# Kernel optimization log

Hardware: AMD Instinct MI355X
Metric: run time of the kernel (lower is better)

Reference implementation:

```python
import jax, jax.numpy as jnp
import numpy as np

B, C, M, T = 2, 512, 16, 128
H = 8
D = C // H  # 64, divisible by 4 for 2D RoPE
G = C // 4  # GroupNorm groups = 128
S = M * T


def group_norm(x, scale, bias, groups=G, eps=1e-5):
    b, c, m, t = x.shape
    xg = x.reshape(b, groups, c // groups, m, t)
    mu = xg.mean(axis=(2, 3, 4), keepdims=True)
    var = xg.var(axis=(2, 3, 4), keepdims=True)
    xn = ((xg - mu) * jax.lax.rsqrt(var + eps)).reshape(b, c, m, t)
    return xn * scale[None, :, None, None] + bias[None, :, None, None]


def dwsep_conv(x, dw, pw):
    # depthwise 3x3 (groups=C) then pointwise 1x1
    y = jax.lax.conv_general_dilated(
        x, dw, window_strides=(1, 1), padding='SAME',
        dimension_numbers=('NCHW', 'HWIO', 'NCHW'), feature_group_count=x.shape[1])
    return jnp.einsum('bcmt,cd->bdmt', y, pw)


def rope2d(x):
    # x: [B,H,M,T,D]; first D/2 dims rotated by freq index m, last D/2 by time index t
    d = x.shape[-1]
    dh = d // 2
    q = dh // 2
    inv = 1.0 / (10000.0 ** (jnp.arange(q, dtype=jnp.float32) / q))

    def rot(v, ang):
        h = v.shape[-1] // 2
        v1, v2 = v[..., :h], v[..., h:]
        c, s = jnp.cos(ang), jnp.sin(ang)
        return jnp.concatenate([v1 * c - v2 * s, v1 * s + v2 * c], axis=-1)

    ang_f = jnp.arange(x.shape[2], dtype=jnp.float32)[:, None] * inv  # [M,q]
    ang_t = jnp.arange(x.shape[3], dtype=jnp.float32)[:, None] * inv  # [T,q]
    xf = rot(x[..., :dh], ang_f[:, None, :])  # broadcast over T
    xt = rot(x[..., dh:], ang_t)
    return jnp.concatenate([xf, xt], axis=-1)


def setup_inputs() -> dict:
    key = jax.random.key(0)
    ks = jax.random.split(key, 14)
    s = 0.02
    return {
        'x': jax.random.normal(ks[0], (B, C, M, T), jnp.float32),
        'lengths': jax.random.randint(ks[1], (B,), T // 2, T + 1),
        'gn_scale': jnp.ones((C,), jnp.float32),
        'gn_bias': jnp.zeros((C,), jnp.float32),
        'dw_q': jax.random.normal(ks[2], (3, 3, 1, C), jnp.float32) * s,
        'dw_k': jax.random.normal(ks[3], (3, 3, 1, C), jnp.float32) * s,
        'dw_v': jax.random.normal(ks[4], (3, 3, 1, C), jnp.float32) * s,
        'pw_q': jax.random.normal(ks[5], (C, C), jnp.float32) * s,
        'pw_k': jax.random.normal(ks[6], (C, C), jnp.float32) * s,
        'pw_v': jax.random.normal(ks[7], (C, C), jnp.float32) * s,
        'attn_w': jax.random.normal(ks[8], (C, C), jnp.float32) * s,
        'attn_b': jnp.zeros((C,), jnp.float32),
        'out_w': jax.random.normal(ks[9], (C, C), jnp.float32) * s,
        'out_b': jnp.zeros((C,), jnp.float32),
    }


def reference(x, lengths, gn_scale, gn_bias, dw_q, dw_k, dw_v, pw_q, pw_k, pw_v,
              attn_w, attn_b, out_w, out_b):
    residual = x
    xn = group_norm(x, gn_scale, gn_bias)

    def to_heads(y):  # [B,C,M,T] -> [B,H,M,T,D]
        return y.reshape(B, H, D, M, T).transpose(0, 1, 3, 4, 2)

    q = rope2d(to_heads(dwsep_conv(xn, dw_q, pw_q)))
    k = rope2d(to_heads(dwsep_conv(xn, dw_k, pw_k)))
    v = to_heads(dwsep_conv(xn, dw_v, pw_v))

    q = q.reshape(B, H, S, D)
    k = k.reshape(B, H, S, D)
    v = v.reshape(B, H, S, D)

    scores = jnp.einsum('bhsd,bhkd->bhsk', q, k) / np.sqrt(D).astype(np.float32)
    valid_t = jnp.arange(T)[None, :] < lengths[:, None]        # [B,T]
    valid = jnp.tile(valid_t, (1, M))                          # [B,S], token idx = m*T + t
    scores = jnp.where(valid[:, None, None, :], scores, jnp.float32(-1e9))
    attn = jax.nn.softmax(scores, axis=-1)
    o = jnp.einsum('bhsk,bhkd->bhsd', attn, v)                 # [B,H,S,D]

    o = o.transpose(0, 2, 1, 3).reshape(B, S, C)
    o = o @ attn_w + attn_b                                    # block output proj
    o = o.reshape(B, M, T, C).transpose(0, 3, 1, 2)            # [B,C,M,T]
    out = jnp.einsum('bcmt,cd->bdmt', o, out_w) + out_b[None, :, None, None]
    return residual + out
```

## Files before the change

kernel.cpp:

```cpp
#include <hip/hip_runtime.h>
#include <math.h>

#define CCH 512
#define SSQ 2048
#define MTOT 4096

typedef __bf16 bf16;
typedef __bf16 bf16x8 __attribute__((ext_vector_type(8)));
typedef __bf16 bf16x4 __attribute__((ext_vector_type(4)));
typedef float  f32x4  __attribute__((ext_vector_type(4)));

#define AS1 __attribute__((address_space(1)))
#define AS3 __attribute__((address_space(3)))
__device__ __forceinline__ void glds16(const void* g, void* l) {
    __builtin_amdgcn_global_load_lds((const AS1 void*)g, (AS3 void*)l, 16, 0, 0);
}

__global__ void gn_stats_kernel(const float* __restrict__ x,
                                float* __restrict__ mu, float* __restrict__ rstd) {
    __shared__ float s_sum[256], s_sq[256];
    int bg = blockIdx.x;
    long base = (long)bg * 8192;
    int tid = threadIdx.x;
    float sum = 0.f, sq = 0.f;
#pragma unroll
    for (int r = 0; r < 32; ++r) {
        float v = x[base + r*256 + tid];
        sum += v; sq += v*v;
    }
    s_sum[tid] = sum; s_sq[tid] = sq;
    __syncthreads();
    for (int off = 128; off > 0; off >>= 1) {
        if (tid < off) { s_sum[tid] += s_sum[tid+off]; s_sq[tid] += s_sq[tid+off]; }
        __syncthreads();
    }
    if (tid == 0) {
        float m = s_sum[0] * (1.f/8192.f);
        float v = s_sq[0]  * (1.f/8192.f) - m*m;
        mu[bg] = m;
        rstd[bg] = rsqrtf(v + 1e-5f);
    }
}

__global__ void wconv_kernel(const float* __restrict__ w0, const float* __restrict__ w1,
                             const float* __restrict__ w2, const float* __restrict__ w3,
                             const float* __restrict__ w4, bf16* __restrict__ out) {
    __shared__ float t[64][65];
    const float* srcs[5] = {w0, w1, w2, w3, w4};
    const float* W = srcs[blockIdx.z];
    bf16* D = out + (long)blockIdx.z * (CCH*CCH);
    int k0 = blockIdx.x*64, n0 = blockIdx.y*64;
    int tid = threadIdx.x;
    int cI = tid & 63, r4 = tid >> 6;
#pragma unroll
    for (int p = 0; p < 16; ++p) {
        int kr = p*4 + r4;
        t[kr][cI] = W[(long)(k0+kr)*CCH + n0 + cI];
    }
    __syncthreads();
#pragma unroll
    for (int p = 0; p < 16; ++p) {
        int nr = p*4 + r4;
        D[(long)(n0+nr)*CCH + k0 + cI] = (bf16)t[cI][nr];
    }
}

__global__ void tn_kernel(const float* __restrict__ x, const float* __restrict__ mu,
                          const float* __restrict__ rstd, const float* __restrict__ gsc,
                          const float* __restrict__ gbs, bf16* __restrict__ xnT) {
    __shared__ float t[64][65];
    int s0 = blockIdx.x*64, c0 = blockIdx.y*64, b = blockIdx.z;
    int tid = threadIdx.x;
    int cI = tid & 63, r4 = tid >> 6;
#pragma unroll
    for (int p = 0; p < 16; ++p) {
        int cr = p*4 + r4;
        t[cr][cI] = x[((long)(b*CCH + c0 + cr))*SSQ + s0 + cI];
    }
    __syncthreads();
#pragma unroll
    for (int p = 0; p < 16; ++p) {
        int sr = p*4 + r4;
        int c = c0 + cI;
        int g = b*128 + (c >> 2);
        float v = (t[cI][sr] - mu[g]) * rstd[g] * gsc[c] + gbs[c];
        xnT[((long)(b*SSQ + s0 + sr))*CCH + c] = (bf16)v;
    }
}

__global__ __launch_bounds__(256) void dw3_kernel(const bf16* __restrict__ xnT,
        const float* __restrict__ dwq, const float* __restrict__ dwk,
        const float* __restrict__ dwv,
        bf16* __restrict__ yq, bf16* __restrict__ yk, bf16* __restrict__ yv) {
    int tid = threadIdx.x;
    int cc = (tid & 63) * 8;
    int s  = blockIdx.x*4 + (tid >> 6);
    int sl = s & (SSQ-1);
    int b  = s >> 11;
    int m = sl >> 7, t = sl & 127;
    float aq[8] = {}, ak[8] = {}, av[8] = {};
#pragma unroll
    for (int di = 0; di < 3; ++di) {
        int m2 = m + di - 1;
        if ((unsigned)m2 >= 16u) continue;
#pragma unroll
        for (int dj = 0; dj < 3; ++dj) {
            int t2 = t + dj - 1;
            if ((unsigned)t2 >= 128u) continue;
            bf16x8 xv = *(const bf16x8*)(xnT + ((long)(b*SSQ + m2*128 + t2))*CCH + cc);
            int wi = (di*3 + dj)*CCH + cc;
#pragma unroll
            for (int i = 0; i < 8; ++i) {
                float xf = (float)xv[i];
                aq[i] += xf * dwq[wi+i];
                ak[i] += xf * dwk[wi+i];
                av[i] += xf * dwv[wi+i];
            }
        }
    }
    bf16x8 oq, ok, ov;
#pragma unroll
    for (int i = 0; i < 8; ++i) { oq[i] = (bf16)aq[i]; ok[i] = (bf16)ak[i]; ov[i] = (bf16)av[i]; }
    long o = (long)s*CCH + cc;
    *(bf16x8*)(yq + o) = oq;
    *(bf16x8*)(yk + o) = ok;
    *(bf16x8*)(yv + o) = ov;
}

template<int MODE>
__global__ __launch_bounds__(256) void gemm_bf16(const bf16* __restrict__ A,
        const bf16* __restrict__ Wt, const float* __restrict__ bias,
        const float* __restrict__ resid, void* __restrict__ outv) {
    __shared__ bf16 As[64*64];
    __shared__ bf16 Bs[64*64];
    int m0 = blockIdx.x*64, n0 = blockIdx.y*64;
    int tid = threadIdx.x, lane = tid & 63, wid = tid >> 6;
    int sw = wid & 1, nw = wid >> 1;
    int col = lane & 15, quad = lane >> 4;
    f32x4 acc[2][2] = {};

    const char* gA[2]; const char* gB[2];
    char* ldsA[2]; char* ldsB[2];
#pragma unroll
    for (int p = 0; p < 2; ++p) {
        int ci = wid*64 + lane + p*256;
        int row = ci >> 3;
        int c = (ci & 7) ^ (row & 7);
        gA[p] = (const char*)A  + ((long)(m0+row)*CCH + c*8)*2;
        gB[p] = (const char*)Wt + ((long)(n0+row)*CCH + c*8)*2;
        ldsA[p] = (char*)As + wid*1024 + p*4096;
        ldsB[p] = (char*)Bs + wid*1024 + p*4096;
    }
    int rowA = sw*32 + col, rowB = nw*32 + col;

    for (int k0 = 0; k0 < CCH; k0 += 64) {
        __syncthreads();
#pragma unroll
        for (int p = 0; p < 2; ++p) {
            glds16(gA[p] + k0*2, ldsA[p]);
            glds16(gB[p] + k0*2, ldsB[p]);
        }
        __syncthreads();
        bf16x8 af[2][2], bf[2][2];
#pragma unroll
        for (int mt = 0; mt < 2; ++mt) {
            int r = rowA + mt*16;
#pragma unroll
            for (int ks = 0; ks < 2; ++ks) {
                int c = (ks*4 + quad) ^ (r & 7);
                af[mt][ks] = *(const bf16x8*)((char*)As + r*128 + c*16);
            }
        }
#pragma unroll
        for (int nt = 0; nt < 2; ++nt) {
            int r = rowB + nt*16;
#pragma unroll
            for (int ks = 0; ks < 2; ++ks) {
                int c = (ks*4 + quad) ^ (r & 7);
                bf[nt][ks] = *(const bf16x8*)((char*)Bs + r*128 + c*16);
            }
        }
#pragma unroll
        for (int ks = 0; ks < 2; ++ks)
#pragma unroll
            for (int mt = 0; mt < 2; ++mt)
#pragma unroll
                for (int nt = 0; nt < 2; ++nt)
                    acc[mt][nt] = __builtin_amdgcn_mfma_f32_16x16x32_bf16(
                        af[mt][ks], bf[nt][ks], acc[mt][nt], 0,0,0);
    }
    int nb = n0 + nw*32;
    int mb = m0 + sw*32;
    if (MODE == 0 || MODE == 1) {
        bf16* outp = (bf16*)outv;
        float invf = __expf(-(float)col * 0.5756462732485114f);
        bool tHalf = (nb & 32) != 0;
        const float sc = (MODE == 0) ? 0.125f : 1.0f;
#pragma unroll
        for (int st = 0; st < 2; ++st)
#pragma unroll
            for (int r = 0; r < 4; ++r) {
                int row = mb + st*16 + quad*4 + r;
                int sl = row & (SSQ-1);
                float pos = tHalf ? (float)(sl & 127) : (float)(sl >> 7);
                float ang = pos * invf;
                float sn, cs;
                __sincosf(ang, &sn, &cs);
                float x1 = acc[st][0][r], x2 = acc[st][1][r];
                outp[(long)row*CCH + nb + col]      = (bf16)((x1*cs - x2*sn)*sc);
                outp[(long)row*CCH + nb + 16 + col] = (bf16)((x1*sn + x2*cs)*sc);
            }
    } else if (MODE == 2) {
        bf16* outp = (bf16*)outv;
#pragma unroll
        for (int st = 0; st < 2; ++st)
#pragma unroll
            for (int nt = 0; nt < 2; ++nt) {
                int n = nb + nt*16 + col;
                int row0 = mb + st*16 + quad*4;
                int b = row0 >> 11, sl0 = row0 & (SSQ-1);
                bf16x4 pk;
#pragma unroll
                for (int r = 0; r < 4; ++r) pk[r] = (bf16)acc[st][nt][r];
                *(bf16x4*)(outp + ((long)(b*CCH + n))*SSQ + sl0) = pk;
            }
    } else if (MODE == 3) {
        bf16* outp = (bf16*)outv;
#pragma unroll
        for (int nt = 0; nt < 2; ++nt) {
            int n = nb + nt*16 + col;
            float bv = bias[n];
#pragma unroll
            for (int st = 0; st < 2; ++st)
#pragma unroll
                for (int r = 0; r < 4; ++r)
                    outp[(long)(mb + st*16 + quad*4 + r)*CCH + n] = (bf16)(acc[st][nt][r] + bv);
        }
    } else {
        float* outp = (float*)outv;
#pragma unroll
        for (int st = 0; st < 2; ++st)
#pragma unroll
            for (int nt = 0; nt < 2; ++nt) {
                int n = nb + nt*16 + col;
                float bv = bias[n];
                int row0 = mb + st*16 + quad*4;
                int b = row0 >> 11, sl0 = row0 & (SSQ-1);
                long off = ((long)(b*CCH + n))*SSQ + sl0;
                float4 rr = *(const float4*)(resid + off);
                float4 o4;
                o4.x = acc[st][nt][0] + bv + rr.x;
                o4.y = acc[st][nt][1] + bv + rr.y;
                o4.z = acc[st][nt][2] + bv + rr.z;
                o4.w = acc[st][nt][3] + bv + rr.w;
                *(float4*)(outp + off) = o4;
            }
    }
}

#define KVROW 88
#define KVIMG (64*KVROW*2)
__global__ __launch_bounds__(256) void attn_kernel(
        const bf16* __restrict__ qb, const bf16* __restrict__ kb,
        const bf16* __restrict__ vb, const int* __restrict__ lengths,
        bf16* __restrict__ o) {
    __shared__ char KVs[2][2*KVIMG];
    __shared__ bf16 Ps[4][16*72];
    int b = blockIdx.z, h = blockIdx.y;
    int tid = threadIdx.x, wid = tid >> 6, lane = tid & 63;
    int col = lane & 15, quad = lane >> 4;
    int q0 = blockIdx.x*64 + wid*16;
    int lenb = lengths[b];

    const char* gp[4]; long gstep[4]; int ldsoff[4];
#pragma unroll
    for (int p = 0; p < 4; ++p) {
        int idx = tid + p*256;
        int isV = idx >> 9;
        int r = (idx >> 3) & 63;
        int c = idx & 7;
        if (!isV) { gp[p] = (const char*)kb + ((long)(b*SSQ + r))*1024 + h*128 + c*16; gstep[p] = 65536; }
        else      { gp[p] = (const char*)vb + ((long)(b*CCH + h*64 + r))*4096 + c*16;  gstep[p] = 128; }
        ldsoff[p] = isV*KVIMG + r*176 + c*16;
    }

    const bf16* qp = qb + (long)(b*SSQ)*CCH + h*64;
    bf16x8 qf[2];
#pragma unroll
    for (int dc = 0; dc < 2; ++dc)
        qf[dc] = *(const bf16x8*)(qp + (long)(q0 + col)*CCH + dc*32 + quad*8);

    f32x4 of[4] = {};
    float lsum = 0.f;
    bf16* pw = Ps[wid];

    bf16x8 sreg[4];
#pragma unroll
    for (int p = 0; p < 4; ++p) sreg[p] = *(const bf16x8*)(gp[p]);
#pragma unroll
    for (int p = 0; p < 4; ++p) *(bf16x8*)(KVs[0] + ldsoff[p]) = sreg[p];
    __syncthreads();

    for (int t = 0; t < 32; ++t) {
        int kt = t*64;
        const bf16* K = (const bf16*)KVs[t & 1];
        const bf16* V = (const bf16*)(KVs[t & 1] + KVIMG);
        if (t < 31) {
#pragma unroll
            for (int p = 0; p < 4; ++p)
                sreg[p] = *(const bf16x8*)(gp[p] + (long)(t+1)*gstep[p]);
        }
        f32x4 acc[4] = {};
#pragma unroll
        for (int sub = 0; sub < 4; ++sub)
#pragma unroll
            for (int dc = 0; dc < 2; ++dc) {
                bf16x8 kf = *(const bf16x8*)(K + (sub*16 + col)*KVROW + dc*32 + quad*8);
                acc[sub] = __builtin_amdgcn_mfma_f32_16x16x32_bf16(kf, qf[dc], acc[sub], 0,0,0);
            }
#pragma unroll
        for (int sub = 0; sub < 4; ++sub) {
            bf16x4 pk;
#pragma unroll
            for (int r = 0; r < 4; ++r) {
                int key = kt + sub*16 + quad*4 + r;
                float p = ((key & 127) < lenb) ? __expf(acc[sub][r]) : 0.f;
                lsum += p;
                pk[r] = (bf16)p;
            }
            *(bf16x4*)(pw + col*72 + sub*16 + quad*4) = pk;
        }
#pragma unroll
        for (int ks = 0; ks < 2; ++ks) {
            bf16x8 pf = *(const bf16x8*)(pw + col*72 + ks*32 + quad*8);
#pragma unroll
            for (int dt = 0; dt < 4; ++dt) {
                bf16x8 vf = *(const bf16x8*)(V + (dt*16 + col)*KVROW + ks*32 + quad*8);
                of[dt] = __builtin_amdgcn_mfma_f32_16x16x32_bf16(pf, vf, of[dt], 0,0,0);
            }
        }
        if (t < 31) {
            char* nb2 = KVs[(t + 1) & 1];
#pragma unroll
            for (int p = 0; p < 4; ++p) *(bf16x8*)(nb2 + ldsoff[p]) = sreg[p];
        }
        __syncthreads();
    }
    lsum += __shfl_xor(lsum, 16);
    lsum += __shfl_xor(lsum, 32);
    float invl = 1.f / lsum;
    float ir[4];
#pragma unroll
    for (int r = 0; r < 4; ++r) ir[r] = __shfl(invl, quad*4 + r);
    bf16* ob = o + (long)(b*SSQ + q0)*CCH + h*64;
#pragma unroll
    for (int dt = 0; dt < 4; ++dt)
#pragma unroll
        for (int r = 0; r < 4; ++r)
            ob[(long)(quad*4 + r)*CCH + dt*16 + col] = (bf16)(of[dt][r] * ir[r]);
}

extern "C" void kernel_launch(void* const* d_in, const int* in_sizes, int n_in,
                              void* d_out, int out_size, void* d_ws, size_t ws_size,
                              hipStream_t stream) {
    const float* x        = (const float*)d_in[0];
    const int*   lengths  = (const int*)  d_in[1];
    const float* gn_scale = (const float*)d_in[2];
    const float* gn_bias  = (const float*)d_in[3];
    const float* dw_q     = (const float*)d_in[4];
    const float* dw_k     = (const float*)d_in[5];
    const float* dw_v     = (const float*)d_in[6];
    const float* pw_q     = (const float*)d_in[7];
    const float* pw_k     = (const float*)d_in[8];
    const float* pw_v     = (const float*)d_in[9];
    const float* attn_w   = (const float*)d_in[10];
    const float* attn_b   = (const float*)d_in[11];
    const float* out_w    = (const float*)d_in[12];
    const float* out_b    = (const float*)d_in[13];
    float* out = (float*)d_out;

    char* w = (char*)d_ws;
    float* mu   = (float*)w;
    float* rstd = (float*)(w + 1024);
    bf16* wT    = (bf16*)(w + 4096);
    bf16* wTq = wT;
    bf16* wTk = wT + 1*CCH*CCH;
    bf16* wTv = wT + 2*CCH*CCH;
    bf16* wTa = wT + 3*CCH*CCH;
    bf16* wTo = wT + 4*CCH*CCH;
    bf16* xnT  = (bf16*)(w + 0x00300000);
    bf16* yqT  = (bf16*)(w + 0x00700000);
    bf16* ykT  = (bf16*)(w + 0x00B00000);
    bf16* yvT  = (bf16*)(w + 0x00F00000);
    bf16* qbf  = (bf16*)(w + 0x01300000);
    bf16* kbf  = (bf16*)(w + 0x01700000);
    bf16* vbf  = (bf16*)(w + 0x01B00000);
    bf16* obf  = (bf16*)(w + 0x01F00000);
    bf16* tmpb = (bf16*)(w + 0x02300000);

    gn_stats_kernel<<<256, 256, 0, stream>>>(x, mu, rstd);
    wconv_kernel<<<dim3(8,8,5), 256, 0, stream>>>(pw_q, pw_k, pw_v, attn_w, out_w, wT);
    tn_kernel<<<dim3(32,8,2), 256, 0, stream>>>(x, mu, rstd, gn_scale, gn_bias, xnT);
    dw3_kernel<<<MTOT/4, 256, 0, stream>>>(xnT, dw_q, dw_k, dw_v, yqT, ykT, yvT);

    dim3 gg(MTOT/64, CCH/64);
    gemm_bf16<0><<<gg, 256, 0, stream>>>(yqT, wTq, nullptr, nullptr, qbf);
    gemm_bf16<1><<<gg, 256, 0, stream>>>(ykT, wTk, nullptr, nullptr, kbf);
    gemm_bf16<2><<<gg, 256, 0, stream>>>(yvT, wTv, nullptr, nullptr, vbf);

    attn_kernel<<<dim3(SSQ/64, 8, 2), 256, 0, stream>>>(qbf, kbf, vbf, lengths, obf);

    gemm_bf16<3><<<gg, 256, 0, stream>>>(obf, wTa, attn_b, nullptr, tmpb);
    gemm_bf16<4><<<gg, 256, 0, stream>>>(tmpb, wTo, out_b, x, out);
}
```

Before: 179.8 us.

## Merge setup kernels, batch QKV GEMMs, and swizzle attention K/V tiles

```diff
diff --git a/kernel.cpp b/kernel.cpp
--- a/kernel.cpp
+++ b/kernel.cpp
@@ -16,52 +16,56 @@
     __builtin_amdgcn_global_load_lds((const AS1 void*)g, (AS3 void*)l, 16, 0, 0);
 }
 
-__global__ void gn_stats_kernel(const float* __restrict__ x,
-                                float* __restrict__ mu, float* __restrict__ rstd) {
-    __shared__ float s_sum[256], s_sq[256];
-    int bg = blockIdx.x;
-    long base = (long)bg * 8192;
+__global__ __launch_bounds__(256) void gnw_kernel(const float* __restrict__ x,
+        float* __restrict__ mu, float* __restrict__ rstd,
+        const float* __restrict__ w0, const float* __restrict__ w1,
+        const float* __restrict__ w2, const float* __restrict__ w3,
+        const float* __restrict__ w4, bf16* __restrict__ wT) {
+    __shared__ float smem[64*65];
     int tid = threadIdx.x;
-    float sum = 0.f, sq = 0.f;
-#pragma unroll
-    for (int r = 0; r < 32; ++r) {
-        float v = x[base + r*256 + tid];
-        sum += v; sq += v*v;
-    }
-    s_sum[tid] = sum; s_sq[tid] = sq;
-    __syncthreads();
-    for (int off = 128; off > 0; off >>= 1) {
-        if (tid < off) { s_sum[tid] += s_sum[tid+off]; s_sq[tid] += s_sq[tid+off]; }
-        __syncthreads();
-    }
-    if (tid == 0) {
-        float m = s_sum[0] * (1.f/8192.f);
-        float v = s_sq[0]  * (1.f/8192.f) - m*m;
-        mu[bg] = m;
-        rstd[bg] = rsqrtf(v + 1e-5f);
-    }
-}
-
-__global__ void wconv_kernel(const float* __restrict__ w0, const float* __restrict__ w1,
-                             const float* __restrict__ w2, const float* __restrict__ w3,
-                             const float* __restrict__ w4, bf16* __restrict__ out) {
-    __shared__ float t[64][65];
-    const float* srcs[5] = {w0, w1, w2, w3, w4};
-    const float* W = srcs[blockIdx.z];
-    bf16* D = out + (long)blockIdx.z * (CCH*CCH);
-    int k0 = blockIdx.x*64, n0 = blockIdx.y*64;
-    int tid = threadIdx.x;
-    int cI = tid & 63, r4 = tid >> 6;
-#pragma unroll
-    for (int p = 0; p < 16; ++p) {
-        int kr = p*4 + r4;
-        t[kr][cI] = W[(long)(k0+kr)*CCH + n0 + cI];
-    }
-    __syncthreads();
-#pragma unroll
-    for (int p = 0; p < 16; ++p) {
-        int nr = p*4 + r4;
-        D[(long)(n0+nr)*CCH + k0 + cI] = (bf16)t[cI][nr];
+    if (blockIdx.x < 256) {
+        float* s_sum = smem;
+        float* s_sq  = smem + 256;
+        int bg = blockIdx.x;
+        long base = (long)bg * 8192;
+        float sum = 0.f, sq = 0.f;
+#pragma unroll
+        for (int r = 0; r < 32; ++r) {
+            float v = x[base + r*256 + tid];
+            sum += v; sq += v*v;
+        }
+        s_sum[tid] = sum; s_sq[tid] = sq;
+        __syncthreads();
+        for (int off = 128; off > 0; off >>= 1) {
+            if (tid < off) { s_sum[tid] += s_sum[tid+off]; s_sq[tid] += s_sq[tid+off]; }
+            __syncthreads();
+        }
+        if (tid == 0) {
+            float m = s_sum[0] * (1.f/8192.f);
+            float v = s_sq[0]  * (1.f/8192.f) - m*m;
+            mu[bg] = m;
+            rstd[bg] = rsqrtf(v + 1e-5f);
+        }
+    } else {
+        int bid = blockIdx.x - 256;
+        int z = bid >> 6, r2 = bid & 63;
+        int k0 = (r2 >> 3)*64, n0 = (r2 & 7)*64;
+        const float* srcs[5] = {w0, w1, w2, w3, w4};
+        const float* W = srcs[z];
+        bf16* D = wT + (long)z * (CCH*CCH);
+        float (*t)[65] = (float(*)[65])smem;
+        int cI = tid & 63, r4 = tid >> 6;
+#pragma unroll
+        for (int p = 0; p < 16; ++p) {
+            int kr = p*4 + r4;
+            t[kr][cI] = W[(long)(k0+kr)*CCH + n0 + cI];
+        }
+        __syncthreads();
+#pragma unroll
+        for (int p = 0; p < 16; ++p) {
+            int nr = p*4 + r4;
+            D[(long)(n0+nr)*CCH + k0 + cI] = (bf16)t[cI][nr];
+        }
     }
 }
 
@@ -127,18 +131,12 @@
     *(bf16x8*)(yv + o) = ov;
 }
 
-template<int MODE>
-__global__ __launch_bounds__(256) void gemm_bf16(const bf16* __restrict__ A,
-        const bf16* __restrict__ Wt, const float* __restrict__ bias,
-        const float* __restrict__ resid, void* __restrict__ outv) {
-    __shared__ bf16 As[64*64];
-    __shared__ bf16 Bs[64*64];
-    int m0 = blockIdx.x*64, n0 = blockIdx.y*64;
+__device__ __forceinline__ void gemm_core(const bf16* __restrict__ A,
+        const bf16* __restrict__ Wt, int m0, int n0,
+        bf16* As, bf16* Bs, f32x4 acc[2][2]) {
     int tid = threadIdx.x, lane = tid & 63, wid = tid >> 6;
     int sw = wid & 1, nw = wid >> 1;
     int col = lane & 15, quad = lane >> 4;
-    f32x4 acc[2][2] = {};
-
     const char* gA[2]; const char* gB[2];
     char* ldsA[2]; char* ldsB[2];
 #pragma unroll
@@ -152,7 +150,6 @@
         ldsB[p] = (char*)Bs + wid*1024 + p*4096;
     }
     int rowA = sw*32 + col, rowB = nw*32 + col;
-
     for (int k0 = 0; k0 < CCH; k0 += 64) {
         __syncthreads();
 #pragma unroll
@@ -161,7 +158,7 @@
             glds16(gB[p] + k0*2, ldsB[p]);
         }
         __syncthreads();
-        bf16x8 af[2][2], bf[2][2];
+        bf16x8 af[2][2], bfr[2][2];
 #pragma unroll
         for (int mt = 0; mt < 2; ++mt) {
             int r = rowA + mt*16;
@@ -177,7 +174,7 @@
 #pragma unroll
             for (int ks = 0; ks < 2; ++ks) {
                 int c = (ks*4 + quad) ^ (r & 7);
-                bf[nt][ks] = *(const bf16x8*)((char*)Bs + r*128 + c*16);
+                bfr[nt][ks] = *(const bf16x8*)((char*)Bs + r*128 + c*16);
             }
         }
 #pragma unroll
@@ -187,15 +184,27 @@
 #pragma unroll
                 for (int nt = 0; nt < 2; ++nt)
                     acc[mt][nt] = __builtin_amdgcn_mfma_f32_16x16x32_bf16(
-                        af[mt][ks], bf[nt][ks], acc[mt][nt], 0,0,0);
-    }
-    int nb = n0 + nw*32;
-    int mb = m0 + sw*32;
-    if (MODE == 0 || MODE == 1) {
-        bf16* outp = (bf16*)outv;
+                        af[mt][ks], bfr[nt][ks], acc[mt][nt], 0,0,0);
+    }
+}
+
+__global__ __launch_bounds__(256) void gemm_qkv(const bf16* __restrict__ Abase,
+        const bf16* __restrict__ wT, bf16* __restrict__ qout,
+        bf16* __restrict__ kout, bf16* __restrict__ vout) {
+    __shared__ bf16 As[64*64];
+    __shared__ bf16 Bs[64*64];
+    int m0 = blockIdx.x*64, n0 = blockIdx.y*64, z = blockIdx.z;
+    f32x4 acc[2][2] = {};
+    gemm_core(Abase + (long)z*MTOT*CCH, wT + (long)z*CCH*CCH, m0, n0, As, Bs, acc);
+    int tid = threadIdx.x, lane = tid & 63, wid = tid >> 6;
+    int sw = wid & 1, nw = wid >> 1;
+    int col = lane & 15, quad = lane >> 4;
+    int nb = n0 + nw*32, mb = m0 + sw*32;
+    if (z < 2) {
+        bf16* outp = z ? kout : qout;
         float invf = __expf(-(float)col * 0.5756462732485114f);
         bool tHalf = (nb & 32) != 0;
-        const float sc = (MODE == 0) ? 0.125f : 1.0f;
+        const float sc = z ? 1.0f : 0.125f;
 #pragma unroll
         for (int st = 0; st < 2; ++st)
 #pragma unroll
@@ -210,8 +219,7 @@
                 outp[(long)row*CCH + nb + col]      = (bf16)((x1*cs - x2*sn)*sc);
                 outp[(long)row*CCH + nb + 16 + col] = (bf16)((x1*sn + x2*cs)*sc);
             }
-    } else if (MODE == 2) {
-        bf16* outp = (bf16*)outv;
+    } else {
 #pragma unroll
         for (int st = 0; st < 2; ++st)
 #pragma unroll
@@ -222,9 +230,25 @@
                 bf16x4 pk;
 #pragma unroll
                 for (int r = 0; r < 4; ++r) pk[r] = (bf16)acc[st][nt][r];
-                *(bf16x4*)(outp + ((long)(b*CCH + n))*SSQ + sl0) = pk;
-            }
-    } else if (MODE == 3) {
+                *(bf16x4*)(vout + ((long)(b*CCH + n))*SSQ + sl0) = pk;
+            }
+    }
+}
+
+template<int MODE>
+__global__ __launch_bounds__(256) void gemm_bf16(const bf16* __restrict__ A,
+        const bf16* __restrict__ Wt, const float* __restrict__ bias,
+        const float* __restrict__ resid, void* __restrict__ outv) {
+    __shared__ bf16 As[64*64];
+    __shared__ bf16 Bs[64*64];
+    int m0 = blockIdx.x*64, n0 = blockIdx.y*64;
+    f32x4 acc[2][2] = {};
+    gemm_core(A, Wt, m0, n0, As, Bs, acc);
+    int tid = threadIdx.x, lane = tid & 63, wid = tid >> 6;
+    int sw = wid & 1, nw = wid >> 1;
+    int col = lane & 15, quad = lane >> 4;
+    int nb = n0 + nw*32, mb = m0 + sw*32;
+    if (MODE == 3) {
         bf16* outp = (bf16*)outv;
 #pragma unroll
         for (int nt = 0; nt < 2; ++nt) {
@@ -258,13 +282,12 @@
     }
 }
 
-#define KVROW 88
-#define KVIMG (64*KVROW*2)
+#define KIMG 8192
 __global__ __launch_bounds__(256) void attn_kernel(
         const bf16* __restrict__ qb, const bf16* __restrict__ kb,
         const bf16* __restrict__ vb, const int* __restrict__ lengths,
         bf16* __restrict__ o) {
-    __shared__ char KVs[2][2*KVIMG];
+    __shared__ char KVs[2*KIMG];
     __shared__ bf16 Ps[4][16*72];
     int b = blockIdx.z, h = blockIdx.y;
     int tid = threadIdx.x, wid = tid >> 6, lane = tid & 63;
@@ -277,12 +300,22 @@
     for (int p = 0; p < 4; ++p) {
         int idx = tid + p*256;
         int isV = idx >> 9;
-        int r = (idx >> 3) & 63;
-        int c = idx & 7;
-        if (!isV) { gp[p] = (const char*)kb + ((long)(b*SSQ + r))*1024 + h*128 + c*16; gstep[p] = 65536; }
-        else      { gp[p] = (const char*)vb + ((long)(b*CCH + h*64 + r))*4096 + c*16;  gstep[p] = 128; }
-        ldsoff[p] = isV*KVIMG + r*176 + c*16;
-    }
+        int rem = idx & 511;
+        int r = rem >> 3;
+        int csrc = (rem & 7) ^ (r & 7);
+        if (!isV) { gp[p] = (const char*)kb + ((long)(b*SSQ + r))*1024 + h*128 + csrc*16; gstep[p] = 65536; }
+        else      { gp[p] = (const char*)vb + ((long)(b*CCH + h*64 + r))*4096 + csrc*16;  gstep[p] = 128; }
+        ldsoff[p] = idx*16;
+    }
+
+    f32x4 vm[2][4];
+#pragma unroll
+    for (int p2 = 0; p2 < 2; ++p2)
+#pragma unroll
+        for (int sub = 0; sub < 4; ++sub)
+#pragma unroll
+            for (int r = 0; r < 4; ++r)
+                vm[p2][sub][r] = (p2*64 + sub*16 + quad*4 + r < lenb) ? 1.f : 0.f;
 
     const bf16* qp = qb + (long)(b*SSQ)*CCH + h*64;
     bf16x8 qf[2];
@@ -293,29 +326,31 @@
     f32x4 of[4] = {};
     float lsum = 0.f;
     bf16* pw = Ps[wid];
+    int cswz = col & 7;
 
     bf16x8 sreg[4];
 #pragma unroll
     for (int p = 0; p < 4; ++p) sreg[p] = *(const bf16x8*)(gp[p]);
-#pragma unroll
-    for (int p = 0; p < 4; ++p) *(bf16x8*)(KVs[0] + ldsoff[p]) = sreg[p];
-    __syncthreads();
 
     for (int t = 0; t < 32; ++t) {
-        int kt = t*64;
-        const bf16* K = (const bf16*)KVs[t & 1];
-        const bf16* V = (const bf16*)(KVs[t & 1] + KVIMG);
+        __syncthreads();
+#pragma unroll
+        for (int p = 0; p < 4; ++p) *(bf16x8*)(KVs + ldsoff[p]) = sreg[p];
+        __syncthreads();
         if (t < 31) {
 #pragma unroll
             for (int p = 0; p < 4; ++p)
                 sreg[p] = *(const bf16x8*)(gp[p] + (long)(t+1)*gstep[p]);
         }
+        const bf16* K = (const bf16*)KVs;
+        const bf16* V = (const bf16*)(KVs + KIMG);
+        int par = t & 1;
         f32x4 acc[4] = {};
 #pragma unroll
         for (int sub = 0; sub < 4; ++sub)
 #pragma unroll
             for (int dc = 0; dc < 2; ++dc) {
-                bf16x8 kf = *(const bf16x8*)(K + (sub*16 + col)*KVROW + dc*32 + quad*8);
+                bf16x8 kf = *(const bf16x8*)((const char*)K + (sub*16 + col)*128 + (((dc*4+quad) ^ cswz))*16);
                 acc[sub] = __builtin_amdgcn_mfma_f32_16x16x32_bf16(kf, qf[dc], acc[sub], 0,0,0);
             }
 #pragma unroll
@@ -323,8 +358,7 @@
             bf16x4 pk;
 #pragma unroll
             for (int r = 0; r < 4; ++r) {
-                int key = kt + sub*16 + quad*4 + r;
-                float p = ((key & 127) < lenb) ? __expf(acc[sub][r]) : 0.f;
+                float p = __expf(acc[sub][r]) * vm[par][sub][r];
                 lsum += p;
                 pk[r] = (bf16)p;
             }
@@ -335,16 +369,10 @@
             bf16x8 pf = *(const bf16x8*)(pw + col*72 + ks*32 + quad*8);
 #pragma unroll
             for (int dt = 0; dt < 4; ++dt) {
-                bf16x8 vf = *(const bf16x8*)(V + (dt*16 + col)*KVROW + ks*32 + quad*8);
+                bf16x8 vf = *(const bf16x8*)((const char*)V + (dt*16 + col)*128 + (((ks*4+quad) ^ cswz))*16);
                 of[dt] = __builtin_amdgcn_mfma_f32_16x16x32_bf16(pf, vf, of[dt], 0,0,0);
             }
         }
-        if (t < 31) {
-            char* nb2 = KVs[(t + 1) & 1];
-#pragma unroll
-            for (int p = 0; p < 4; ++p) *(bf16x8*)(nb2 + ldsoff[p]) = sreg[p];
-        }
-        __syncthreads();
     }
     lsum += __shfl_xor(lsum, 16);
     lsum += __shfl_xor(lsum, 32);
@@ -383,33 +411,26 @@
     float* mu   = (float*)w;
     float* rstd = (float*)(w + 1024);
     bf16* wT    = (bf16*)(w + 4096);
-    bf16* wTq = wT;
-    bf16* wTk = wT + 1*CCH*CCH;
-    bf16* wTv = wT + 2*CCH*CCH;
     bf16* wTa = wT + 3*CCH*CCH;
     bf16* wTo = wT + 4*CCH*CCH;
     bf16* xnT  = (bf16*)(w + 0x00300000);
-    bf16* yqT  = (bf16*)(w + 0x00700000);
-    bf16* ykT  = (bf16*)(w + 0x00B00000);
-    bf16* yvT  = (bf16*)(w + 0x00F00000);
+    bf16* yT   = (bf16*)(w + 0x00700000);
     bf16* qbf  = (bf16*)(w + 0x01300000);
     bf16* kbf  = (bf16*)(w + 0x01700000);
     bf16* vbf  = (bf16*)(w + 0x01B00000);
     bf16* obf  = (bf16*)(w + 0x01F00000);
     bf16* tmpb = (bf16*)(w + 0x02300000);
 
-    gn_stats_kernel<<<256, 256, 0, stream>>>(x, mu, rstd);
-    wconv_kernel<<<dim3(8,8,5), 256, 0, stream>>>(pw_q, pw_k, pw_v, attn_w, out_w, wT);
+    gnw_kernel<<<576, 256, 0, stream>>>(x, mu, rstd, pw_q, pw_k, pw_v, attn_w, out_w, wT);
     tn_kernel<<<dim3(32,8,2), 256, 0, stream>>>(x, mu, rstd, gn_scale, gn_bias, xnT);
-    dw3_kernel<<<MTOT/4, 256, 0, stream>>>(xnT, dw_q, dw_k, dw_v, yqT, ykT, yvT);
+    dw3_kernel<<<MTOT/4, 256, 0, stream>>>(xnT, dw_q, dw_k, dw_v,
+                                           yT, yT + (long)MTOT*CCH, yT + (long)2*MTOT*CCH);
+
+    gemm_qkv<<<dim3(MTOT/64, CCH/64, 3), 256, 0, stream>>>(yT, wT, qbf, kbf, vbf);
+
+    attn_kernel<<<dim3(SSQ/64, 8, 2), 256, 0, stream>>>(qbf, kbf, vbf, lengths, obf);
 
     dim3 gg(MTOT/64, CCH/64);
-    gemm_bf16<0><<<gg, 256, 0, stream>>>(yqT, wTq, nullptr, nullptr, qbf);
-    gemm_bf16<1><<<gg, 256, 0, stream>>>(ykT, wTk, nullptr, nullptr, kbf);
-    gemm_bf16<2><<<gg, 256, 0, stream>>>(yvT, wTv, nullptr, nullptr, vbf);
-
-    attn_kernel<<<dim3(SSQ/64, 8, 2), 256, 0, stream>>>(qbf, kbf, vbf, lengths, obf);
-
     gemm_bf16<3><<<gg, 256, 0, stream>>>(obf, wTa, attn_b, nullptr, tmpb);
     gemm_bf16<4><<<gg, 256, 0, stream>>>(tmpb, wTo, out_b, x, out);
 }
```

After: 164.6 us. 8.5% less time.
